# Optimization experiments

Measured on AMD Instinct MI355X. Metric: run time of the kernel, lower is better.

The kernel has to match this reference:

```python
import jax, jax.numpy as jnp
import numpy as np

B, L, D, NH, NP = 8, 4096, 384, 8, 4


def setup_inputs() -> dict:
    key = jax.random.key(0)
    ks = jax.random.split(key, 16)
    s = 1.0 / np.sqrt(D)
    f32 = jnp.float32
    inp = {
        'query': jax.random.normal(ks[0], (B, L, D), f32),
        'key':   jax.random.normal(ks[1], (B, L, D), f32),
        'value': jax.random.normal(ks[2], (B, L, D), f32),
        # linear weights stored as [in, out]; x @ W + b
        'Wq': jax.random.normal(ks[3], (D, D), f32) * s,
        'bq': jnp.zeros((D,), f32),
        'Wk': jax.random.normal(ks[4], (D, D), f32) * s,
        'bk': jnp.zeros((D,), f32),
        'Wv': jax.random.normal(ks[5], (D, D), f32) * s,
        'bv': jnp.zeros((D,), f32),
        'Woff': jax.random.normal(ks[6], (D, NH * NP * 2), f32) * s,
        'boff': jnp.zeros((NH * NP * 2,), f32),
        'Wwt': jax.random.normal(ks[7], (D, NH * NP), f32) * s,
        'bwt': jnp.zeros((NH * NP,), f32),
        'Wo': jax.random.normal(ks[8], (D, D), f32) * s,
        'bo': jnp.zeros((D,), f32),
        'num_heads': NH,
        'n_points': NP,
    }
    return inp


def reference(query, key, value, Wq, bq, Wk, bk, Wv, bv, Woff, boff, Wwt, bwt, Wo, bo, num_heads, n_points):
    Bq, Lq, Dm = query.shape
    Lk = key.shape[1]
    Lv = value.shape[1]
    hd = Dm // num_heads
    h = w = int(round(np.sqrt(Lk)))  # original: feature_size = int(sqrt(Lk))

    q = query @ Wq + bq          # computed as in original (only its reshape is used via output path)
    k = key @ Wk + bk            # faithful: k_proj is computed but unused downstream
    v = value @ Wv + bv

    # offsets [B, nH, Lq, nP, 2] and softmax point weights [B, nH, Lq, nP]
    off = (query @ Woff + boff).reshape(Bq, Lq, num_heads, n_points, 2).transpose(0, 2, 1, 3, 4)
    wt = jax.nn.softmax((query @ Wwt + bwt).reshape(Bq, Lq, num_heads, n_points).transpose(0, 2, 1, 3), axis=-1)

    # reference grid: ref[...,0] = x (tiled over rows), ref[...,1] = y (repeated over cols)
    yy = jnp.linspace(0.0, 1.0, h)
    xx = jnp.linspace(0.0, 1.0, w)
    gy, gx = jnp.meshgrid(yy, xx, indexing='ij')
    ref = jnp.stack([gx.reshape(-1), gy.reshape(-1)], axis=-1)  # [L, 2]

    loc = jnp.clip(ref[None, None, :, None, :] + off, 0.0, 1.0)  # [B,nH,Lq,nP,2]
    # NOTE: faithful to source, which multiplies component 0 by (h-1) (its 'h' coord)
    ph = loc[..., 0] * (h - 1)   # row pixel coord, in [0, h-1]
    pw = loc[..., 1] * (w - 1)   # col pixel coord, in [0, w-1]

    y0 = jnp.floor(ph)
    x0 = jnp.floor(pw)
    wy = (ph - y0)[..., None]
    wx = (pw - x0)[..., None]
    y0i = y0.astype(jnp.int32)
    x0i = x0.astype(jnp.int32)
    y1i = jnp.minimum(y0i + 1, h - 1)
    x1i = jnp.minimum(x0i + 1, w - 1)

    vh = v.reshape(Bq, Lv, num_heads, hd).transpose(0, 2, 1, 3)  # [B,nH,Lv,hd]

    def gather(yi, xi):
        idx = (yi * w + xi).reshape(Bq, num_heads, Lq * n_points, 1)
        return jnp.take_along_axis(vh, idx, axis=2).reshape(Bq, num_heads, Lq, n_points, hd)

    # bilinear sample (align_corners=True; coords in-range so zero-padding never triggers)
    sampled = ((1 - wy) * ((1 - wx) * gather(y0i, x0i) + wx * gather(y0i, x1i))
               + wy * ((1 - wx) * gather(y1i, x0i) + wx * gather(y1i, x1i)))

    out = jnp.einsum('bhlp,bhlpd->bhld', wt, sampled)  # weighted point aggregation
    out = out.transpose(0, 2, 1, 3).reshape(Bq, Lq, Dm)
    return out @ Wo + bo  # dropout is identity in eval mode
```

## Files before the change

### kernel.cpp

```cpp
#include <hip/hip_runtime.h>
#include <hip/hip_bf16.h>
#include <stdint.h>

using bf16 = __hip_bfloat16;

typedef __attribute__((ext_vector_type(8))) short short8;
typedef __attribute__((ext_vector_type(4))) float float4v;

namespace {
constexpr int kL  = 4096;
constexpr int kD  = 384;
constexpr int kGW = 64;
constexpr int kM  = 32768;
constexpr int kAP = 392;

constexpr size_t nValue = (size_t)kM * kD;
constexpr size_t nW     = (size_t)kD * kD;
constexpr size_t nWcat  = (size_t)96 * kD;

constexpr size_t oWvt  = 0;
constexpr size_t oWot  = oWvt  + nW * 2;
constexpr size_t oWch  = oWot  + nW * 2;
constexpr size_t oWcl  = oWch  + nWcat * 2;
constexpr size_t oBcat = oWcl  + nWcat * 2;
constexpr size_t oVB   = (oBcat + 96 * 4 + 255) & ~size_t(255);
constexpr size_t oProj = oVB   + nValue * 2;
}

__device__ __forceinline__ void load_lds_16(const void* g, void* l) {
  __builtin_amdgcn_global_load_lds((const __attribute__((address_space(1))) void*)g,
                                   (__attribute__((address_space(3))) void*)l,
                                   16, 0, 0);
}

__device__ __forceinline__ short bf16bits(float f) {
  bf16 h = __float2bfloat16(f);
  return *reinterpret_cast<short*>(&h);
}

__device__ __forceinline__ float bf16raw2f(unsigned short u) {
  union { unsigned int i; float f; } c;
  c.i = ((unsigned int)u) << 16;
  return c.f;
}

__global__ void prep_kernel(const float* __restrict__ Wv,
                            const float* __restrict__ Wo,
                            const float* __restrict__ Woff,
                            const float* __restrict__ Wwt,
                            const float* __restrict__ boff,
                            const float* __restrict__ bwt,
                            bf16* __restrict__ Wvt, bf16* __restrict__ Wot,
                            bf16* __restrict__ Wch, bf16* __restrict__ Wcl,
                            float* __restrict__ bcat)
{
  size_t i = (size_t)blockIdx.x * 256 + threadIdx.x;
  if (i < nW) {
    const int n = (int)(i / kD), k = (int)(i % kD);
    Wvt[i] = __float2bfloat16(Wv[(size_t)k * kD + n]);
    return;
  }
  i -= nW;
  if (i < nW) {
    const int n = (int)(i / kD), k = (int)(i % kD);
    Wot[i] = __float2bfloat16(Wo[(size_t)k * kD + n]);
    return;
  }
  i -= nW;
  if (i < nWcat) {
    const int n = (int)(i / kD), k = (int)(i % kD);
    const float val = (n < 64) ? Woff[(size_t)k * 64 + n] : Wwt[(size_t)k * 32 + (n - 64)];
    const bf16 h = __float2bfloat16(val);
    Wch[i] = h;
    Wcl[i] = __float2bfloat16(val - __bfloat162float(h));
    return;
  }
  i -= nWcat;
  if (i < 96) bcat[i] = (i < 64) ? boff[i] : bwt[i - 64];
}

__device__ __forceinline__
void vgemm_body(char* smem, int bid,
                const float* __restrict__ A, const bf16* __restrict__ Bt,
                const float* __restrict__ bias, bf16* __restrict__ Cout)
{
  bf16* sA = (bf16*)smem;
  bf16* sB = (bf16*)(smem + 16384);
  const int tid  = threadIdx.x;
  const int lane = tid & 63;
  const int wave = tid >> 6;
  const int bm = bid / 3, bn = bid % 3;
  const int m0 = bm * 128, n0 = bn * 128;
  const int wm = (wave >> 1) * 64, wn = (wave & 1) * 64;
  const int r16 = lane & 15, quad = lane >> 4;

  float4v acc[4][4];
  #pragma unroll
  for (int i = 0; i < 4; ++i)
    #pragma unroll
    for (int j = 0; j < 4; ++j) acc[i][j] = (float4v){0.f, 0.f, 0.f, 0.f};

  const int c0 = tid, c1 = tid + 256;
  const int rA0 = c0 >> 2, cA0 = c0 & 3;
  const int rA1 = c1 >> 2, cA1 = c1 & 3;

  float4 f00, f01, f10, f11;

  {
    const float* s0 = A + (size_t)(m0 + rA0) * kD + cA0 * 8;
    f00 = *(const float4*)s0; f01 = *(const float4*)(s0 + 4);
    const float* s1 = A + (size_t)(m0 + rA1) * kD + cA1 * 8;
    f10 = *(const float4*)s1; f11 = *(const float4*)(s1 + 4);
    load_lds_16(Bt + (size_t)(n0 + rA0) * kD + cA0 * 8, (char*)sB + c0 * 16);
    load_lds_16(Bt + (size_t)(n0 + rA1) * kD + cA1 * 8, (char*)sB + c1 * 16);
    short8 hx;
    hx[0]=bf16bits(f00.x); hx[1]=bf16bits(f00.y); hx[2]=bf16bits(f00.z); hx[3]=bf16bits(f00.w);
    hx[4]=bf16bits(f01.x); hx[5]=bf16bits(f01.y); hx[6]=bf16bits(f01.z); hx[7]=bf16bits(f01.w);
    *(short8*)((char*)sA + c0 * 16) = hx;
    hx[0]=bf16bits(f10.x); hx[1]=bf16bits(f10.y); hx[2]=bf16bits(f10.z); hx[3]=bf16bits(f10.w);
    hx[4]=bf16bits(f11.x); hx[5]=bf16bits(f11.y); hx[6]=bf16bits(f11.z); hx[7]=bf16bits(f11.w);
    *(short8*)((char*)sA + c1 * 16) = hx;
  }
  __syncthreads();

  for (int kt = 0; kt < 12; ++kt) {
    const int cur = kt & 1, nxt = cur ^ 1;
    if (kt < 11) {
      const int k0n = (kt + 1) * 32;
      const float* s0 = A + (size_t)(m0 + rA0) * kD + k0n + cA0 * 8;
      f00 = *(const float4*)s0; f01 = *(const float4*)(s0 + 4);
      const float* s1 = A + (size_t)(m0 + rA1) * kD + k0n + cA1 * 8;
      f10 = *(const float4*)s1; f11 = *(const float4*)(s1 + 4);
      load_lds_16(Bt + (size_t)(n0 + rA0) * kD + k0n + cA0 * 8, (char*)sB + nxt * 8192 + c0 * 16);
      load_lds_16(Bt + (size_t)(n0 + rA1) * kD + k0n + cA1 * 8, (char*)sB + nxt * 8192 + c1 * 16);
    }
    const bf16* sAc = (const bf16*)((char*)sA + cur * 8192);
    const bf16* sBc = (const bf16*)((char*)sB + cur * 8192);
    short8 av[4], bv[4];
    #pragma unroll
    for (int i = 0; i < 4; ++i)
      av[i] = *(const short8*)(sAc + (wm + i * 16 + r16) * 32 + quad * 8);
    #pragma unroll
    for (int j = 0; j < 4; ++j)
      bv[j] = *(const short8*)(sBc + (wn + j * 16 + r16) * 32 + quad * 8);
    #pragma unroll
    for (int i = 0; i < 4; ++i)
      #pragma unroll
      for (int j = 0; j < 4; ++j)
        acc[i][j] = __builtin_amdgcn_mfma_f32_16x16x32_bf16(av[i], bv[j], acc[i][j], 0, 0, 0);
    if (kt < 11) {
      short8 hx;
      hx[0]=bf16bits(f00.x); hx[1]=bf16bits(f00.y); hx[2]=bf16bits(f00.z); hx[3]=bf16bits(f00.w);
      hx[4]=bf16bits(f01.x); hx[5]=bf16bits(f01.y); hx[6]=bf16bits(f01.z); hx[7]=bf16bits(f01.w);
      *(short8*)((char*)sA + nxt * 8192 + c0 * 16) = hx;
      hx[0]=bf16bits(f10.x); hx[1]=bf16bits(f10.y); hx[2]=bf16bits(f10.z); hx[3]=bf16bits(f10.w);
      hx[4]=bf16bits(f11.x); hx[5]=bf16bits(f11.y); hx[6]=bf16bits(f11.z); hx[7]=bf16bits(f11.w);
      *(short8*)((char*)sA + nxt * 8192 + c1 * 16) = hx;
      __syncthreads();
    }
  }

  #pragma unroll
  for (int j = 0; j < 4; ++j) {
    const int col = n0 + wn + j * 16 + r16;
    const float bj = bias[col];
    #pragma unroll
    for (int i = 0; i < 4; ++i) {
      const int mbase = m0 + wm + i * 16 + quad * 4;
      #pragma unroll
      for (int r = 0; r < 4; ++r)
        Cout[(size_t)(mbase + r) * kD + col] = __float2bfloat16(acc[i][j][r] + bj);
    }
  }
}

__device__ __forceinline__
void proj_body(char* smem, int bid,
               const float* __restrict__ Q,
               const bf16* __restrict__ WhT, const bf16* __restrict__ WlT,
               const float* __restrict__ bc, float* __restrict__ proj)
{
  bf16* sAh  = (bf16*)smem;
  bf16* sAl  = (bf16*)(smem + 16384);
  char* sBhB = smem + 32768;
  char* sBlB = smem + 45056;
  const int tid  = threadIdx.x;
  const int lane = tid & 63;
  const int wave = tid >> 6;
  const int m0 = bid * 128;
  const int wm = (wave >> 1) * 64, wn = (wave & 1) * 48;
  const int r16 = lane & 15, quad = lane >> 4;

  float4v acc[4][3];
  #pragma unroll
  for (int i = 0; i < 4; ++i)
    #pragma unroll
    for (int j = 0; j < 3; ++j) acc[i][j] = (float4v){0.f, 0.f, 0.f, 0.f};

  const int c0 = tid, c1 = tid + 256;
  const int rA0 = c0 >> 2, cA0 = c0 & 3;
  const int rA1 = c1 >> 2, cA1 = c1 & 3;
  const int cB1 = tid + 256;
  const int cB2 = tid + 128;

  float4 f00, f01, f10, f11;

  auto stageB = [&](int k0, int buf) {
    load_lds_16(WhT + (size_t)(tid >> 2) * kD + k0 + (tid & 3) * 8, sBhB + buf * 6144 + tid * 16);
    if (cB1 < 384) {
      load_lds_16(WhT + (size_t)(cB1 >> 2) * kD + k0 + (cB1 & 3) * 8, sBhB + buf * 6144 + cB1 * 16);
    } else {
      const int cc = cB1 - 384;
      load_lds_16(WlT + (size_t)(cc >> 2) * kD + k0 + (cc & 3) * 8, sBlB + buf * 6144 + cc * 16);
    }
    load_lds_16(WlT + (size_t)(cB2 >> 2) * kD + k0 + (cB2 & 3) * 8, sBlB + buf * 6144 + cB2 * 16);
  };
  auto castA = [&](int buf) {
    const float fv0[8] = {f00.x, f00.y, f00.z, f00.w, f01.x, f01.y, f01.z, f01.w};
    const float fv1[8] = {f10.x, f10.y, f10.z, f10.w, f11.x, f11.y, f11.z, f11.w};
    short8 hx, lx;
    #pragma unroll
    for (int q = 0; q < 8; ++q) {
      const bf16 h = __float2bfloat16(fv0[q]);
      hx[q] = *reinterpret_cast<const short*>(&h);
      const bf16 lo = __float2bfloat16(fv0[q] - __bfloat162float(h));
      lx[q] = *reinterpret_cast<const short*>(&lo);
    }
    *(short8*)((char*)sAh + buf * 8192 + c0 * 16) = hx;
    *(short8*)((char*)sAl + buf * 8192 + c0 * 16) = lx;
    #pragma unroll
    for (int q = 0; q < 8; ++q) {
      const bf16 h = __float2bfloat16(fv1[q]);
      hx[q] = *reinterpret_cast<const short*>(&h);
      const bf16 lo = __float2bfloat16(fv1[q] - __bfloat162float(h));
      lx[q] = *reinterpret_cast<const short*>(&lo);
    }
    *(short8*)((char*)sAh + buf * 8192 + c1 * 16) = hx;
    *(short8*)((char*)sAl + buf * 8192 + c1 * 16) = lx;
  };
  auto loadA = [&](int k0) {
    const float* s0 = Q + (size_t)(m0 + rA0) * kD + k0 + cA0 * 8;
    f00 = *(const float4*)s0; f01 = *(const float4*)(s0 + 4);
    const float* s1 = Q + (size_t)(m0 + rA1) * kD + k0 + cA1 * 8;
    f10 = *(const float4*)s1; f11 = *(const float4*)(s1 + 4);
  };

  loadA(0);
  stageB(0, 0);
  castA(0);
  __syncthreads();

  for (int kt = 0; kt < 12; ++kt) {
    const int cur = kt & 1, nxt = cur ^ 1;
    if (kt < 11) {
      loadA((kt + 1) * 32);
      stageB((kt + 1) * 32, nxt);
    }
    const bf16* sAhc = (const bf16*)((char*)sAh + cur * 8192);
    const bf16* sAlc = (const bf16*)((char*)sAl + cur * 8192);
    const bf16* sBhc = (const bf16*)(sBhB + cur * 6144);
    const bf16* sBlc = (const bf16*)(sBlB + cur * 6144);
    short8 avh[4], avl[4];
    #pragma unroll
    for (int i = 0; i < 4; ++i) {
      avh[i] = *(const short8*)(sAhc + (wm + i * 16 + r16) * 32 + quad * 8);
      avl[i] = *(const short8*)(sAlc + (wm + i * 16 + r16) * 32 + quad * 8);
    }
    #pragma unroll
    for (int j = 0; j < 3; ++j) {
      const short8 bvh = *(const short8*)(sBhc + (wn + j * 16 + r16) * 32 + quad * 8);
      const short8 bvl = *(const short8*)(sBlc + (wn + j * 16 + r16) * 32 + quad * 8);
      #pragma unroll
      for (int i = 0; i < 4; ++i) {
        acc[i][j] = __builtin_amdgcn_mfma_f32_16x16x32_bf16(avh[i], bvh, acc[i][j], 0, 0, 0);
        acc[i][j] = __builtin_amdgcn_mfma_f32_16x16x32_bf16(avh[i], bvl, acc[i][j], 0, 0, 0);
        acc[i][j] = __builtin_amdgcn_mfma_f32_16x16x32_bf16(avl[i], bvh, acc[i][j], 0, 0, 0);
      }
    }
    if (kt < 11) {
      castA(nxt);
      __syncthreads();
    }
  }

  #pragma unroll
  for (int j = 0; j < 3; ++j) {
    const int col = wn + j * 16 + r16;
    const float bj = bc[col];
    #pragma unroll
    for (int i = 0; i < 4; ++i) {
      const int mbase = m0 + wm + i * 16 + quad * 4;
      #pragma unroll
      for (int r = 0; r < 4; ++r)
        proj[(size_t)(mbase + r) * 96 + col] = acc[i][j][r] + bj;
    }
  }
}

__global__ __launch_bounds__(256)
void fat_kernel(const float* __restrict__ value, const bf16* __restrict__ Wvt,
                const float* __restrict__ bv,    bf16* __restrict__ vB,
                const float* __restrict__ Q,     const bf16* __restrict__ Wch,
                const bf16* __restrict__ Wcl,    const float* __restrict__ bcat,
                float* __restrict__ proj)
{
  __shared__ __align__(16) char smem[57344];
  const int pb = blockIdx.x;
  if (pb < 256) {
    proj_body(smem, pb, Q, Wch, Wcl, bcat, proj);
  } else {
    vgemm_body(smem, pb - 256, value, Wvt, bv, vB);
  }
}

__global__ __launch_bounds__(512)
void tail_kernel(const float* __restrict__ proj, const bf16* __restrict__ v,
                 const bf16* __restrict__ Wot, const float* __restrict__ bo,
                 float* __restrict__ out)
{
  __shared__ __align__(16) char smem[149504];
  bf16* sAgg = (bf16*)smem;
  char* aux  = smem + 100352;
  int4*   scoff = (int4*)aux;
  float4* scw   = (float4*)(aux + 16384);
  char*   sBB   = aux;

  const int raw   = blockIdx.x;
  const int chunk = (raw & 7) * 32 + (raw >> 3);
  const int m0    = chunk * 128;
  const int b     = m0 >> 12;
  const int l0    = m0 & 4095;
  const int t     = threadIdx.x;

  for (int qt = 0; qt < 4; ++qt) {
    const int tok0 = qt * 32;
    #pragma unroll
    for (int it = 0; it < 2; ++it) {
      const int task = t + it * 512;
      const int tl   = task >> 5;
      const int pt   = task & 31;
      const int tok  = tok0 + tl;
      const int l    = l0 + tok;
      const float* pb_ = proj + (size_t)(m0 + tok) * 96;
      const float2 off = *(const float2*)(pb_ + 2 * pt);
      const int h = pt >> 2, p = pt & 3;
      const float4 lg = *(const float4*)(pb_ + 64 + h * 4);
      const float g[4] = {lg.x, lg.y, lg.z, lg.w};
      const float mx = fmaxf(fmaxf(g[0], g[1]), fmaxf(g[2], g[3]));
      float e[4], sum = 0.f;
      #pragma unroll
      for (int jj = 0; jj < 4; ++jj) { e[jj] = expf(g[jj] - mx); sum += e[jj]; }
      const float wt = e[p] / sum;
      const float refx = (float)(l & 63) * (1.0f / 63.0f);
      const float refy = (float)(l >> 6) * (1.0f / 63.0f);
      const float locx = fminf(fmaxf(refx + off.x, 0.f), 1.f);
      const float locy = fminf(fmaxf(refy + off.y, 0.f), 1.f);
      const float ph = locx * 63.0f;
      const float pw = locy * 63.0f;
      const float fy = floorf(ph), fx = floorf(pw);
      const int y0 = (int)fy, x0 = (int)fx;
      const int y1 = min(y0 + 1, 63), x1 = min(x0 + 1, 63);
      const float wy = ph - fy, wx = pw - fx;
      scoff[tl * 32 + pt] = make_int4((y0 * kGW + x0) * kD, (y0 * kGW + x1) * kD,
                                      (y1 * kGW + x0) * kD, (y1 * kGW + x1) * kD);
      scw[tl * 32 + pt] = make_float4(wt * (1.f - wy) * (1.f - wx), wt * (1.f - wy) * wx,
                                      wt * wy * (1.f - wx),         wt * wy * wx);
    }
    __syncthreads();
    #pragma unroll
    for (int it = 0; it < 6; ++it) {
      const int task = t + it * 512;
      const int tl = task / 96;
      const int q  = task - tl * 96;
      const int h  = q / 12;
      const int col = q * 4;
      const unsigned short* vb = (const unsigned short*)(v + (size_t)b * kL * kD + col);
      float4v acc = (float4v){0.f, 0.f, 0.f, 0.f};
      #pragma unroll
      for (int p = 0; p < 4; ++p) {
        const int4   o = scoff[tl * 32 + h * 4 + p];
        const float4 w = scw  [tl * 32 + h * 4 + p];
        const ushort4 u0 = *(const ushort4*)(vb + o.x);
        const ushort4 u1 = *(const ushort4*)(vb + o.y);
        const ushort4 u2 = *(const ushort4*)(vb + o.z);
        const ushort4 u3 = *(const ushort4*)(vb + o.w);
        acc[0] += w.x * bf16raw2f(u0.x) + w.y * bf16raw2f(u1.x)
                + w.z * bf16raw2f(u2.x) + w.w * bf16raw2f(u3.x);
        acc[1] += w.x * bf16raw2f(u0.y) + w.y * bf16raw2f(u1.y)
                + w.z * bf16raw2f(u2.y) + w.w * bf16raw2f(u3.y);
        acc[2] += w.x * bf16raw2f(u0.z) + w.y * bf16raw2f(u1.z)
                + w.z * bf16raw2f(u2.z) + w.w * bf16raw2f(u3.z);
        acc[3] += w.x * bf16raw2f(u0.w) + w.y * bf16raw2f(u1.w)
                + w.z * bf16raw2f(u2.w) + w.w * bf16raw2f(u3.w);
      }
      ushort4 ou;
      ou.x = (unsigned short)bf16bits(acc[0]);
      ou.y = (unsigned short)bf16bits(acc[1]);
      ou.z = (unsigned short)bf16bits(acc[2]);
      ou.w = (unsigned short)bf16bits(acc[3]);
      *(ushort4*)(sAgg + (size_t)(tok0 + tl) * kAP + col) = ou;
    }
    __syncthreads();
  }

  const int lane = t & 63, wave = t >> 6;
  const int r16 = lane & 15, quad = lane >> 4;
  const int wm = (wave >> 2) * 64;
  const int wn = (wave & 3) * 96;
  float4v acc2[4][6];
  #pragma unroll
  for (int i = 0; i < 4; ++i)
    #pragma unroll
    for (int j = 0; j < 6; ++j) acc2[i][j] = (float4v){0.f, 0.f, 0.f, 0.f};

  #pragma unroll
  for (int r = 0; r < 3; ++r) {
    const int c = t + r * 512;
    load_lds_16(Wot + (size_t)(c >> 2) * kD + (c & 3) * 8, sBB + c * 16);
  }
  __syncthreads();

  for (int kt = 0; kt < 12; ++kt) {
    const int cur = kt & 1;
    if (kt < 11) {
      const int k0n = (kt + 1) * 32;
      #pragma unroll
      for (int r = 0; r < 3; ++r) {
        const int c = t + r * 512;
        load_lds_16(Wot + (size_t)(c >> 2) * kD + k0n + (c & 3) * 8,
                    sBB + (cur ^ 1) * 24576 + c * 16);
      }
    }
    const int k0 = kt * 32;
    const bf16* sBc = (const bf16*)(sBB + cur * 24576);
    short8 av[4];
    #pragma unroll
    for (int i = 0; i < 4; ++i)
      av[i] = *(const short8*)(sAgg + (size_t)(wm + i * 16 + r16) * kAP + k0 + quad * 8);
    #pragma unroll
    for (int j = 0; j < 6; ++j) {
      const short8 bvj = *(const short8*)(sBc + (wn + j * 16 + r16) * 32 + quad * 8);
      #pragma unroll
      for (int i = 0; i < 4; ++i)
        acc2[i][j] = __builtin_amdgcn_mfma_f32_16x16x32_bf16(av[i], bvj, acc2[i][j], 0, 0, 0);
    }
    if (kt < 11) __syncthreads();
  }

  #pragma unroll
  for (int j = 0; j < 6; ++j) {
    const int col = wn + j * 16 + r16;
    const float bj = bo[col];
    #pragma unroll
    for (int i = 0; i < 4; ++i) {
      const int mb = m0 + wm + i * 16 + quad * 4;
      #pragma unroll
      for (int r = 0; r < 4; ++r)
        out[(size_t)(mb + r) * kD + col] = acc2[i][j][r] + bj;
    }
  }
}

extern "C" void kernel_launch(void* const* d_in, const int* in_sizes, int n_in,
                              void* d_out, int out_size, void* d_ws, size_t ws_size,
                              hipStream_t stream)
{
  const float* query = (const float*)d_in[0];
  const float* value = (const float*)d_in[2];
  const float* Wv    = (const float*)d_in[7];
  const float* bv    = (const float*)d_in[8];
  const float* Woff  = (const float*)d_in[9];
  const float* boff  = (const float*)d_in[10];
  const float* Wwt   = (const float*)d_in[11];
  const float* bwt   = (const float*)d_in[12];
  const float* Wo    = (const float*)d_in[13];
  const float* bo    = (const float*)d_in[14];
  float* out = (float*)d_out;

  char* ws = (char*)d_ws;
  bf16*  Wvt  = (bf16*)(ws + oWvt);
  bf16*  Wot  = (bf16*)(ws + oWot);
  bf16*  Wch  = (bf16*)(ws + oWch);
  bf16*  Wcl  = (bf16*)(ws + oWcl);
  float* bcat = (float*)(ws + oBcat);
  bf16*  vB   = (bf16*)(ws + oVB);
  float* proj = (float*)(ws + oProj);

  const size_t prepN = nW + nW + nWcat + 96;
  prep_kernel<<<dim3((unsigned)((prepN + 255) / 256)), 256, 0, stream>>>(
      Wv, Wo, Woff, Wwt, boff, bwt, Wvt, Wot, Wch, Wcl, bcat);

  fat_kernel<<<dim3(256 + 768), 256, 0, stream>>>(
      value, Wvt, bv, vB, query, Wch, Wcl, bcat, proj);

  tail_kernel<<<dim3(256), 512, 0, stream>>>(proj, vB, Wot, bo, out);
}
```

Before: 269.9 us.

## Drop LDS staging in GEMMs, load MFMA operands directly from global

The value and offset/weight projection GEMMs now read MFMA fragments straight from global memory, converting fp32 to bf16 in registers, instead of staging double-buffered tiles through LDS with barriers. The tail kernel halves its tile to 64 tokens per block with twice as many blocks, uses a smaller LDS footprint, and reads Wo fragments directly from global. This is meant to remove LDS traffic and barriers and to raise occupancy. In exchange it gives up data reuse across waves and issues row-strided global loads that coalesce poorly, relying on L1/L2 to absorb the redundant reads.

New measurement: 312.2 us. +15.6%, slower.

```diff
diff --git a/kernel.cpp b/kernel.cpp
--- a/kernel.cpp
+++ b/kernel.cpp
@@ -27,12 +27,6 @@
 constexpr size_t oProj = oVB   + nValue * 2;
 }
 
-__device__ __forceinline__ void load_lds_16(const void* g, void* l) {
-  __builtin_amdgcn_global_load_lds((const __attribute__((address_space(1))) void*)g,
-                                   (__attribute__((address_space(3))) void*)l,
-                                   16, 0, 0);
-}
-
 __device__ __forceinline__ short bf16bits(float f) {
   bf16 h = __float2bfloat16(f);
   return *reinterpret_cast<short*>(&h);
@@ -42,6 +36,27 @@
   union { unsigned int i; float f; } c;
   c.i = ((unsigned int)u) << 16;
   return c.f;
+}
+
+__device__ __forceinline__ short8 pack_hi8(const float4& f0, const float4& f1) {
+  short8 hx;
+  hx[0] = bf16bits(f0.x); hx[1] = bf16bits(f0.y);
+  hx[2] = bf16bits(f0.z); hx[3] = bf16bits(f0.w);
+  hx[4] = bf16bits(f1.x); hx[5] = bf16bits(f1.y);
+  hx[6] = bf16bits(f1.z); hx[7] = bf16bits(f1.w);
+  return hx;
+}
+
+__device__ __forceinline__ void pack_hilo8(const float4& f0, const float4& f1,
+                                           short8& hx, short8& lx) {
+  const float fv[8] = {f0.x, f0.y, f0.z, f0.w, f1.x, f1.y, f1.z, f1.w};
+  #pragma unroll
+  for (int q = 0; q < 8; ++q) {
+    const bf16 h = __float2bfloat16(fv[q]);
+    hx[q] = *reinterpret_cast<const short*>(&h);
+    const bf16 lo = __float2bfloat16(fv[q] - __bfloat162float(h));
+    lx[q] = *reinterpret_cast<const short*>(&lo);
+  }
 }
 
 __global__ void prep_kernel(const float* __restrict__ Wv,
@@ -80,12 +95,9 @@
 }
 
 __device__ __forceinline__
-void vgemm_body(char* smem, int bid,
-                const float* __restrict__ A, const bf16* __restrict__ Bt,
+void vgemm_body(int bid, const float* __restrict__ A, const bf16* __restrict__ Bt,
                 const float* __restrict__ bias, bf16* __restrict__ Cout)
 {
-  bf16* sA = (bf16*)smem;
-  bf16* sB = (bf16*)(smem + 16384);
   const int tid  = threadIdx.x;
   const int lane = tid & 63;
   const int wave = tid >> 6;
@@ -100,64 +112,26 @@
     #pragma unroll
     for (int j = 0; j < 4; ++j) acc[i][j] = (float4v){0.f, 0.f, 0.f, 0.f};
 
-  const int c0 = tid, c1 = tid + 256;
-  const int rA0 = c0 >> 2, cA0 = c0 & 3;
-  const int rA1 = c1 >> 2, cA1 = c1 & 3;
-
-  float4 f00, f01, f10, f11;
-
-  {
-    const float* s0 = A + (size_t)(m0 + rA0) * kD + cA0 * 8;
-    f00 = *(const float4*)s0; f01 = *(const float4*)(s0 + 4);
-    const float* s1 = A + (size_t)(m0 + rA1) * kD + cA1 * 8;
-    f10 = *(const float4*)s1; f11 = *(const float4*)(s1 + 4);
-    load_lds_16(Bt + (size_t)(n0 + rA0) * kD + cA0 * 8, (char*)sB + c0 * 16);
-    load_lds_16(Bt + (size_t)(n0 + rA1) * kD + cA1 * 8, (char*)sB + c1 * 16);
-    short8 hx;
-    hx[0]=bf16bits(f00.x); hx[1]=bf16bits(f00.y); hx[2]=bf16bits(f00.z); hx[3]=bf16bits(f00.w);
-    hx[4]=bf16bits(f01.x); hx[5]=bf16bits(f01.y); hx[6]=bf16bits(f01.z); hx[7]=bf16bits(f01.w);
-    *(short8*)((char*)sA + c0 * 16) = hx;
-    hx[0]=bf16bits(f10.x); hx[1]=bf16bits(f10.y); hx[2]=bf16bits(f10.z); hx[3]=bf16bits(f10.w);
-    hx[4]=bf16bits(f11.x); hx[5]=bf16bits(f11.y); hx[6]=bf16bits(f11.z); hx[7]=bf16bits(f11.w);
-    *(short8*)((char*)sA + c1 * 16) = hx;
-  }
-  __syncthreads();
-
+  const float* Abase = A  + (size_t)(m0 + wm + r16) * kD + quad * 8;
+  const bf16*  Bbase = Bt + (size_t)(n0 + wn + r16) * kD + quad * 8;
+
+  #pragma unroll
   for (int kt = 0; kt < 12; ++kt) {
-    const int cur = kt & 1, nxt = cur ^ 1;
-    if (kt < 11) {
-      const int k0n = (kt + 1) * 32;
-      const float* s0 = A + (size_t)(m0 + rA0) * kD + k0n + cA0 * 8;
-      f00 = *(const float4*)s0; f01 = *(const float4*)(s0 + 4);
-      const float* s1 = A + (size_t)(m0 + rA1) * kD + k0n + cA1 * 8;
-      f10 = *(const float4*)s1; f11 = *(const float4*)(s1 + 4);
-      load_lds_16(Bt + (size_t)(n0 + rA0) * kD + k0n + cA0 * 8, (char*)sB + nxt * 8192 + c0 * 16);
-      load_lds_16(Bt + (size_t)(n0 + rA1) * kD + k0n + cA1 * 8, (char*)sB + nxt * 8192 + c1 * 16);
-    }
-    const bf16* sAc = (const bf16*)((char*)sA + cur * 8192);
-    const bf16* sBc = (const bf16*)((char*)sB + cur * 8192);
+    const int k0 = kt * 32;
     short8 av[4], bv[4];
     #pragma unroll
-    for (int i = 0; i < 4; ++i)
-      av[i] = *(const short8*)(sAc + (wm + i * 16 + r16) * 32 + quad * 8);
+    for (int i = 0; i < 4; ++i) {
+      const float* pa = Abase + (size_t)(i * 16) * kD + k0;
+      av[i] = pack_hi8(*(const float4*)pa, *(const float4*)(pa + 4));
+    }
     #pragma unroll
     for (int j = 0; j < 4; ++j)
-      bv[j] = *(const short8*)(sBc + (wn + j * 16 + r16) * 32 + quad * 8);
+      bv[j] = *(const short8*)(Bbase + (size_t)(j * 16) * kD + k0);
     #pragma unroll
     for (int i = 0; i < 4; ++i)
       #pragma unroll
       for (int j = 0; j < 4; ++j)
         acc[i][j] = __builtin_amdgcn_mfma_f32_16x16x32_bf16(av[i], bv[j], acc[i][j], 0, 0, 0);
-    if (kt < 11) {
-      short8 hx;
-      hx[0]=bf16bits(f00.x); hx[1]=bf16bits(f00.y); hx[2]=bf16bits(f00.z); hx[3]=bf16bits(f00.w);
-      hx[4]=bf16bits(f01.x); hx[5]=bf16bits(f01.y); hx[6]=bf16bits(f01.z); hx[7]=bf16bits(f01.w);
-      *(short8*)((char*)sA + nxt * 8192 + c0 * 16) = hx;
-      hx[0]=bf16bits(f10.x); hx[1]=bf16bits(f10.y); hx[2]=bf16bits(f10.z); hx[3]=bf16bits(f10.w);
-      hx[4]=bf16bits(f11.x); hx[5]=bf16bits(f11.y); hx[6]=bf16bits(f11.z); hx[7]=bf16bits(f11.w);
-      *(short8*)((char*)sA + nxt * 8192 + c1 * 16) = hx;
-      __syncthreads();
-    }
   }
 
   #pragma unroll
@@ -175,15 +149,10 @@
 }
 
 __device__ __forceinline__
-void proj_body(char* smem, int bid,
-               const float* __restrict__ Q,
+void proj_body(int bid, const float* __restrict__ Q,
                const bf16* __restrict__ WhT, const bf16* __restrict__ WlT,
                const float* __restrict__ bc, float* __restrict__ proj)
 {
-  bf16* sAh  = (bf16*)smem;
-  bf16* sAl  = (bf16*)(smem + 16384);
-  char* sBhB = smem + 32768;
-  char* sBlB = smem + 45056;
   const int tid  = threadIdx.x;
   const int lane = tid & 63;
   const int wave = tid >> 6;
@@ -197,89 +166,29 @@
     #pragma unroll
     for (int j = 0; j < 3; ++j) acc[i][j] = (float4v){0.f, 0.f, 0.f, 0.f};
 
-  const int c0 = tid, c1 = tid + 256;
-  const int rA0 = c0 >> 2, cA0 = c0 & 3;
-  const int rA1 = c1 >> 2, cA1 = c1 & 3;
-  const int cB1 = tid + 256;
-  const int cB2 = tid + 128;
-
-  float4 f00, f01, f10, f11;
-
-  auto stageB = [&](int k0, int buf) {
-    load_lds_16(WhT + (size_t)(tid >> 2) * kD + k0 + (tid & 3) * 8, sBhB + buf * 6144 + tid * 16);
-    if (cB1 < 384) {
-      load_lds_16(WhT + (size_t)(cB1 >> 2) * kD + k0 + (cB1 & 3) * 8, sBhB + buf * 6144 + cB1 * 16);
-    } else {
-      const int cc = cB1 - 384;
-      load_lds_16(WlT + (size_t)(cc >> 2) * kD + k0 + (cc & 3) * 8, sBlB + buf * 6144 + cc * 16);
-    }
-    load_lds_16(WlT + (size_t)(cB2 >> 2) * kD + k0 + (cB2 & 3) * 8, sBlB + buf * 6144 + cB2 * 16);
-  };
-  auto castA = [&](int buf) {
-    const float fv0[8] = {f00.x, f00.y, f00.z, f00.w, f01.x, f01.y, f01.z, f01.w};
-    const float fv1[8] = {f10.x, f10.y, f10.z, f10.w, f11.x, f11.y, f11.z, f11.w};
-    short8 hx, lx;
-    #pragma unroll
-    for (int q = 0; q < 8; ++q) {
-      const bf16 h = __float2bfloat16(fv0[q]);
-      hx[q] = *reinterpret_cast<const short*>(&h);
-      const bf16 lo = __float2bfloat16(fv0[q] - __bfloat162float(h));
-      lx[q] = *reinterpret_cast<const short*>(&lo);
-    }
-    *(short8*)((char*)sAh + buf * 8192 + c0 * 16) = hx;
-    *(short8*)((char*)sAl + buf * 8192 + c0 * 16) = lx;
-    #pragma unroll
-    for (int q = 0; q < 8; ++q) {
-      const bf16 h = __float2bfloat16(fv1[q]);
-      hx[q] = *reinterpret_cast<const short*>(&h);
-      const bf16 lo = __float2bfloat16(fv1[q] - __bfloat162float(h));
-      lx[q] = *reinterpret_cast<const short*>(&lo);
-    }
-    *(short8*)((char*)sAh + buf * 8192 + c1 * 16) = hx;
-    *(short8*)((char*)sAl + buf * 8192 + c1 * 16) = lx;
-  };
-  auto loadA = [&](int k0) {
-    const float* s0 = Q + (size_t)(m0 + rA0) * kD + k0 + cA0 * 8;
-    f00 = *(const float4*)s0; f01 = *(const float4*)(s0 + 4);
-    const float* s1 = Q + (size_t)(m0 + rA1) * kD + k0 + cA1 * 8;
-    f10 = *(const float4*)s1; f11 = *(const float4*)(s1 + 4);
-  };
-
-  loadA(0);
-  stageB(0, 0);
-  castA(0);
-  __syncthreads();
-
+  const float* Abase  = Q   + (size_t)(m0 + wm + r16) * kD + quad * 8;
+  const bf16*  Bhbase = WhT + (size_t)(wn + r16) * kD + quad * 8;
+  const bf16*  Blbase = WlT + (size_t)(wn + r16) * kD + quad * 8;
+
+  #pragma unroll
   for (int kt = 0; kt < 12; ++kt) {
-    const int cur = kt & 1, nxt = cur ^ 1;
-    if (kt < 11) {
-      loadA((kt + 1) * 32);
-      stageB((kt + 1) * 32, nxt);
-    }
-    const bf16* sAhc = (const bf16*)((char*)sAh + cur * 8192);
-    const bf16* sAlc = (const bf16*)((char*)sAl + cur * 8192);
-    const bf16* sBhc = (const bf16*)(sBhB + cur * 6144);
-    const bf16* sBlc = (const bf16*)(sBlB + cur * 6144);
+    const int k0 = kt * 32;
     short8 avh[4], avl[4];
     #pragma unroll
     for (int i = 0; i < 4; ++i) {
-      avh[i] = *(const short8*)(sAhc + (wm + i * 16 + r16) * 32 + quad * 8);
-      avl[i] = *(const short8*)(sAlc + (wm + i * 16 + r16) * 32 + quad * 8);
+      const float* pa = Abase + (size_t)(i * 16) * kD + k0;
+      pack_hilo8(*(const float4*)pa, *(const float4*)(pa + 4), avh[i], avl[i]);
     }
     #pragma unroll
     for (int j = 0; j < 3; ++j) {
-      const short8 bvh = *(const short8*)(sBhc + (wn + j * 16 + r16) * 32 + quad * 8);
-      const short8 bvl = *(const short8*)(sBlc + (wn + j * 16 + r16) * 32 + quad * 8);
+      const short8 bvh = *(const short8*)(Bhbase + (size_t)(j * 16) * kD + k0);
+      const short8 bvl = *(const short8*)(Blbase + (size_t)(j * 16) * kD + k0);
       #pragma unroll
       for (int i = 0; i < 4; ++i) {
         acc[i][j] = __builtin_amdgcn_mfma_f32_16x16x32_bf16(avh[i], bvh, acc[i][j], 0, 0, 0);
         acc[i][j] = __builtin_amdgcn_mfma_f32_16x16x32_bf16(avh[i], bvl, acc[i][j], 0, 0, 0);
         acc[i][j] = __builtin_amdgcn_mfma_f32_16x16x32_bf16(avl[i], bvh, acc[i][j], 0, 0, 0);
       }
-    }
-    if (kt < 11) {
-      castA(nxt);
-      __syncthreads();
     }
   }
 
@@ -304,12 +213,11 @@
                 const bf16* __restrict__ Wcl,    const float* __restrict__ bcat,
                 float* __restrict__ proj)
 {
-  __shared__ __align__(16) char smem[57344];
   const int pb = blockIdx.x;
   if (pb < 256) {
-    proj_body(smem, pb, Q, Wch, Wcl, bcat, proj);
+    proj_body(pb, Q, Wch, Wcl, bcat, proj);
   } else {
-    vgemm_body(smem, pb - 256, value, Wvt, bv, vB);
+    vgemm_body(pb - 256, value, Wvt, bv, vB);
   }
 }
 
@@ -318,29 +226,24 @@
                  const bf16* __restrict__ Wot, const float* __restrict__ bo,
                  float* __restrict__ out)
 {
-  __shared__ __align__(16) char smem[149504];
-  bf16* sAgg = (bf16*)smem;
-  char* aux  = smem + 100352;
-  int4*   scoff = (int4*)aux;
-  float4* scw   = (float4*)(aux + 16384);
-  char*   sBB   = aux;
+  __shared__ __align__(16) char smem[66560];
+  bf16*   sAgg  = (bf16*)smem;
+  int4*   scoff = (int4*)(smem + 50176);
+  float4* scw   = (float4*)(smem + 58368);
 
   const int raw   = blockIdx.x;
-  const int chunk = (raw & 7) * 32 + (raw >> 3);
-  const int m0    = chunk * 128;
+  const int chunk = (raw & 7) * 64 + (raw >> 3);
+  const int m0    = chunk * 64;
   const int b     = m0 >> 12;
   const int l0    = m0 & 4095;
   const int t     = threadIdx.x;
 
-  for (int qt = 0; qt < 4; ++qt) {
-    const int tok0 = qt * 32;
-    #pragma unroll
-    for (int it = 0; it < 2; ++it) {
-      const int task = t + it * 512;
-      const int tl   = task >> 5;
-      const int pt   = task & 31;
-      const int tok  = tok0 + tl;
-      const int l    = l0 + tok;
+  for (int ct = 0; ct < 4; ++ct) {
+    const int tok0 = ct * 16;
+    {
+      const int tl = t >> 5, pt = t & 31;
+      const int tok = tok0 + tl;
+      const int l   = l0 + tok;
       const float* pb_ = proj + (size_t)(m0 + tok) * 96;
       const float2 off = *(const float2*)(pb_ + 2 * pt);
       const int h = pt >> 2, p = pt & 3;
@@ -368,7 +271,7 @@
     }
     __syncthreads();
     #pragma unroll
-    for (int it = 0; it < 6; ++it) {
+    for (int it = 0; it < 3; ++it) {
       const int task = t + it * 512;
       const int tl = task / 96;
       const int q  = task - tl * 96;
@@ -405,55 +308,38 @@
 
   const int lane = t & 63, wave = t >> 6;
   const int r16 = lane & 15, quad = lane >> 4;
-  const int wm = (wave >> 2) * 64;
-  const int wn = (wave & 3) * 96;
-  float4v acc2[4][6];
+  const int wn = wave * 48;
+  float4v acc2[4][3];
   #pragma unroll
   for (int i = 0; i < 4; ++i)
     #pragma unroll
-    for (int j = 0; j < 6; ++j) acc2[i][j] = (float4v){0.f, 0.f, 0.f, 0.f};
-
-  #pragma unroll
-  for (int r = 0; r < 3; ++r) {
-    const int c = t + r * 512;
-    load_lds_16(Wot + (size_t)(c >> 2) * kD + (c & 3) * 8, sBB + c * 16);
-  }
-  __syncthreads();
-
+    for (int j = 0; j < 3; ++j) acc2[i][j] = (float4v){0.f, 0.f, 0.f, 0.f};
+
+  const bf16* Bbase = Wot + (size_t)(wn + r16) * kD + quad * 8;
+
+  #pragma unroll
   for (int kt = 0; kt < 12; ++kt) {
-    const int cur = kt & 1;
-    if (kt < 11) {
-      const int k0n = (kt + 1) * 32;
-      #pragma unroll
-      for (int r = 0; r < 3; ++r) {
-        const int c = t + r * 512;
-        load_lds_16(Wot + (size_t)(c >> 2) * kD + k0n + (c & 3) * 8,
-                    sBB + (cur ^ 1) * 24576 + c * 16);
-      }
-    }
     const int k0 = kt * 32;
-    const bf16* sBc = (const bf16*)(sBB + cur * 24576);
     short8 av[4];
     #pragma unroll
     for (int i = 0; i < 4; ++i)
-      av[i] = *(const short8*)(sAgg + (size_t)(wm + i * 16 + r16) * kAP + k0 + quad * 8);
-    #pragma unroll
-    for (int j = 0; j < 6; ++j) {
-      const short8 bvj = *(const short8*)(sBc + (wn + j * 16 + r16) * 32 + quad * 8);
+      av[i] = *(const short8*)(sAgg + (size_t)(i * 16 + r16) * kAP + k0 + quad * 8);
+    #pragma unroll
+    for (int j = 0; j < 3; ++j) {
+      const short8 bvj = *(const short8*)(Bbase + (size_t)(j * 16) * kD + k0);
       #pragma unroll
       for (int i = 0; i < 4; ++i)
         acc2[i][j] = __builtin_amdgcn_mfma_f32_16x16x32_bf16(av[i], bvj, acc2[i][j], 0, 0, 0);
     }
-    if (kt < 11) __syncthreads();
-  }
-
-  #pragma unroll
-  for (int j = 0; j < 6; ++j) {
+  }
+
+  #pragma unroll
+  for (int j = 0; j < 3; ++j) {
     const int col = wn + j * 16 + r16;
     const float bj = bo[col];
     #pragma unroll
     for (int i = 0; i < 4; ++i) {
-      const int mb = m0 + wm + i * 16 + quad * 4;
+      const int mb = m0 + i * 16 + quad * 4;
       #pragma unroll
       for (int r = 0; r < 4; ++r)
         out[(size_t)(mb + r) * kD + col] = acc2[i][j][r] + bj;
@@ -493,5 +379,5 @@
   fat_kernel<<<dim3(256 + 768), 256, 0, stream>>>(
       value, Wvt, bv, vB, query, Wch, Wcl, bcat, proj);
 
-  tail_kernel<<<dim3(256), 512, 0, stream>>>(proj, vB, Wot, bo, out);
-}
+  tail_kernel<<<dim3(512), 512, 0, stream>>>(proj, vB, Wot, bo, out);
+}
```
